# Performance work log

Measured on AMD Instinct MI355X. Metric: run time of the kernel, lower is better.

Reference implementation:

```python
import jax, jax.numpy as jnp
import numpy as np

LEAKY_ALPHA = 0.2
LN_EPS = 1e-5


def setup_inputs() -> dict:
    key = jax.random.key(0)
    ks = jax.random.split(key, 6)
    B, N, D, R, Hh, hd = 2, 2048, 128, 3, 4, 32  # head_dim = out_dim // num_heads = 128 // 4
    H = jax.random.normal(ks[0], (B, N, D), dtype=jnp.float32)
    A = jax.random.randint(ks[1], (R, B, N, N), 0, 2, dtype=jnp.int32)  # 0/1 adjacency per relation
    w_scale = float(np.sqrt(2.0 / (D + hd)))  # xavier-like
    a_scale = float(np.sqrt(2.0 / (hd + 1)))
    W = jax.random.normal(ks[2], (R, Hh, D, hd), dtype=jnp.float32) * w_scale
    a_src = jax.random.normal(ks[3], (R, Hh, hd), dtype=jnp.float32) * a_scale
    a_dst = jax.random.normal(ks[4], (R, Hh, hd), dtype=jnp.float32) * a_scale
    ln_gamma = jnp.ones((D,), dtype=jnp.float32)
    ln_beta = jnp.zeros((D,), dtype=jnp.float32)
    return {"H": H, "A": A, "W": W, "a_src": a_src, "a_dst": a_dst,
            "ln_gamma": ln_gamma, "ln_beta": ln_beta}


def reference(H, A, W, a_src, a_dst, ln_gamma, ln_beta):
    # H: [B,N,D]; A: [R,B,N,N] int; W: [R,Hh,D,hd]; a_*: [R,Hh,hd]
    R = W.shape[0]
    B, N, D = H.shape
    mask = (A > 0)[:, :, None, :, :]                    # [R,B,1,N,N]
    Wh = jnp.einsum('bnd,rhdf->rbhnf', H, W)             # [R,B,Hh,N,hd]
    e_src = jnp.einsum('rbhnf,rhf->rbhn', Wh, a_src)
    e_dst = jnp.einsum('rbhnf,rhf->rbhn', Wh, a_dst)
    e = e_src[..., :, None] + e_dst[..., None, :]        # [R,B,Hh,N,N]
    e = jax.nn.leaky_relu(e, LEAKY_ALPHA)
    all_false = ~jnp.any(mask, axis=-1, keepdims=True)   # rows with empty neighborhood
    logits = jnp.where(mask, e, -jnp.inf)
    logits = jnp.where(all_false, 0.0, logits)           # avoid NaN on empty rows
    alpha = jax.nn.softmax(logits, axis=-1)
    alpha = jnp.where(all_false, 0.0, alpha)
    # attention-weighted aggregation, mean over relations; -> [B,N,Hh,hd]
    agg = jnp.einsum('rbhij,rbhjf->bihf', alpha, Wh) / R
    out = agg.reshape(B, N, -1)                          # concat heads -> [B,N,out_dim]
    x = H + out                                          # res_proj is Identity (in_dim==out_dim); dropout in eval
    mu = jnp.mean(x, axis=-1, keepdims=True)
    var = jnp.var(x, axis=-1, keepdims=True)
    return (x - mu) / jnp.sqrt(var + LN_EPS) * ln_gamma + ln_beta
```

## Files before the change

### kernel.cpp

```cpp
#include <hip/hip_runtime.h>
#include <hip/hip_bf16.h>

#define RR 3
#define BB 2
#define NN 2048
#define DD 128
#define HH 4
#define HD 32
#define LEAKY 0.2f
#define LN_EPS 1e-5f
#define LOG2E 1.4426950408889634f

using f32x4  = __attribute__((ext_vector_type(4))) float;
using bf16x8 = __attribute__((ext_vector_type(8))) short;

__device__ __forceinline__ void gload_lds16(const void* g, void* l) {
    __builtin_amdgcn_global_load_lds(
        (const __attribute__((address_space(1))) unsigned*)g,
        (__attribute__((address_space(3))) unsigned*)l, 16, 0, 0);
}
__device__ __forceinline__ void gload_lds4(const void* g, void* l) {
    __builtin_amdgcn_global_load_lds(
        (const __attribute__((address_space(1))) unsigned*)g,
        (__attribute__((address_space(3))) unsigned*)l, 4, 0, 0);
}
__device__ __forceinline__ unsigned short bfb(float x) {
    return __builtin_bit_cast(unsigned short, __float2bfloat16(x));
}

__global__ __launch_bounds__(256) void prep_kernel(
    const float* __restrict__ H, const int* __restrict__ A,
    const float* __restrict__ W,
    const float* __restrict__ a_src, const float* __restrict__ a_dst,
    float* __restrict__ es, float* __restrict__ ed,
    __hip_bfloat16* __restrict__ whT, unsigned* __restrict__ bm)
{
    const int bid = blockIdx.x;
    const int t = threadIdx.x;

    if (bid >= 384) {
        const int cb = bid - 384;
        const int wave = cb * 4 + (t >> 6);
        const int lane = t & 63;
        const long base = (long)wave * 2048;
        const int* Ap = A + base;
        unsigned word = 0;
#pragma unroll
        for (int e = 0; e < 32; ++e) {
            const int v = Ap[e * 64 + lane];
            const unsigned long long bal = __ballot(v != 0);
            if ((lane >> 1) == e)
                word = (lane & 1) ? (unsigned)(bal >> 32) : (unsigned)bal;
        }
        bm[(base >> 5) + lane] = word;
        return;
    }

    const int rbh = bid >> 4;
    const int nch = bid & 15;
    const int h = rbh & 3;
    const int b = (rbh >> 2) & 1;
    const int r = rbh >> 3;
    const int wi = r * HH + h;
    const int w  = t >> 6;
    const int l  = t & 63;
    const int lr = l & 15;
    const int lg = l >> 4;

    const float* Wp = W + (long)wi * DD * HD;
    bf16x8 afr[2][4];
#pragma unroll
    for (int mt = 0; mt < 2; ++mt)
#pragma unroll
        for (int kt = 0; kt < 4; ++kt)
#pragma unroll
            for (int e = 0; e < 8; ++e)
                afr[mt][kt][e] = (short)bfb(Wp[(kt * 32 + lg * 8 + e) * HD + mt * 16 + lr]);

    float av[2][4], dv[2][4];
#pragma unroll
    for (int mt = 0; mt < 2; ++mt)
#pragma unroll
        for (int reg = 0; reg < 4; ++reg) {
            const int f = mt * 16 + lg * 4 + reg;
            av[mt][reg] = a_src[wi * HD + f] * LOG2E;
            dv[mt][reg] = a_dst[wi * HD + f] * LOG2E;
        }

#pragma unroll
    for (int nt = 0; nt < 2; ++nt) {
        const int ncol = nch * 128 + w * 32 + nt * 16 + lr;
        const float4* hrow4 = (const float4*)(H + ((long)b * NN + ncol) * DD);
        f32x4 acc0 = {0.f, 0.f, 0.f, 0.f};
        f32x4 acc1 = {0.f, 0.f, 0.f, 0.f};
#pragma unroll
        for (int kt = 0; kt < 4; ++kt) {
            float4 h0 = hrow4[kt * 8 + lg * 2];
            float4 h1 = hrow4[kt * 8 + lg * 2 + 1];
            bf16x8 bfr;
            bfr[0] = (short)bfb(h0.x); bfr[1] = (short)bfb(h0.y);
            bfr[2] = (short)bfb(h0.z); bfr[3] = (short)bfb(h0.w);
            bfr[4] = (short)bfb(h1.x); bfr[5] = (short)bfb(h1.y);
            bfr[6] = (short)bfb(h1.z); bfr[7] = (short)bfb(h1.w);
            acc0 = __builtin_amdgcn_mfma_f32_16x16x32_bf16(afr[0][kt], bfr, acc0, 0, 0, 0);
            acc1 = __builtin_amdgcn_mfma_f32_16x16x32_bf16(afr[1][kt], bfr, acc1, 0, 0, 0);
        }
        float s = 0.f, d = 0.f;
#pragma unroll
        for (int reg = 0; reg < 4; ++reg) {
            const int f0 = lg * 4 + reg;
            const int f1 = 16 + lg * 4 + reg;
            whT[((long)rbh * HD + f0) * NN + ncol] = __float2bfloat16(acc0[reg]);
            whT[((long)rbh * HD + f1) * NN + ncol] = __float2bfloat16(acc1[reg]);
            s = fmaf(acc0[reg], av[0][reg], s);
            s = fmaf(acc1[reg], av[1][reg], s);
            d = fmaf(acc0[reg], dv[0][reg], d);
            d = fmaf(acc1[reg], dv[1][reg], d);
        }
        s += __shfl_xor(s, 16); s += __shfl_xor(s, 32);
        d += __shfl_xor(d, 16); d += __shfl_xor(d, 32);
        if (l < 16) {
            es[(long)rbh * NN + ncol] = s;
            ed[(long)rbh * NN + ncol] = d;
        }
    }
}

__global__ __launch_bounds__(256, 3) void gat_attn_kernel(
    const unsigned* __restrict__ bm, const float* __restrict__ es,
    const float* __restrict__ ed, const __hip_bfloat16* __restrict__ whT,
    unsigned* __restrict__ num, float* __restrict__ den)
{
    const int lg = ((int)blockIdx.x % 8) * 96 + (int)blockIdx.x / 8;
    const int jh = lg & 1;
    const int it = (lg >> 1) & 15;
    const int h  = (lg >> 5) & 3;
    const int b  = (lg >> 7) & 1;
    const int r  = lg >> 8;
    const int i0 = it << 7;
    const int tid = threadIdx.x;
    const int w = tid >> 6;
    const int l = tid & 63;
    const int row = l & 15;
    const int kg  = l >> 4;
    const int f31 = l & 31;
    const int kgr = l >> 5;

    __shared__ __align__(16) short    whs[2][4][4][32][8];
    __shared__ __align__(16) unsigned bms[2][4][128];
    __shared__ __align__(16) float    eds[2][4][32];
    __shared__ float red[4];

    const int rbh = (r * BB + b) * HH + h;
    const long rbNN = (long)(r * BB + b) * NN;
    const __hip_bfloat16* whTr = whT + (long)rbh * HD * NN;
    const float* edr = ed + (long)rbh * NN;
    const int jbase = jh * (NN / 2);

#define STAGE(s, nb) do {                                                           \
        const int j0s = jbase + (s) * 128;                                          \
        gload_lds16(whTr + (long)f31 * NN + j0s + w * 32 + kgr * 8,                 \
                    &whs[nb][w][0][0][0]);                                          \
        gload_lds16(whTr + (long)f31 * NN + j0s + w * 32 + (2 + kgr) * 8,           \
                    &whs[nb][w][2][0][0]);                                          \
        gload_lds4(bm + (rbNN + i0 + l) * (NN / 32) + (j0s >> 5) + w,               \
                   &bms[nb][w][0]);                                                 \
        gload_lds4(bm + (rbNN + i0 + 64 + l) * (NN / 32) + (j0s >> 5) + w,          \
                   &bms[nb][w][64]);                                                \
        if (l < 32) gload_lds4(edr + j0s + w * 32 + l, &eds[nb][w][0]);             \
    } while (0)

    STAGE(0, 0);

    float4 m0 = ((const float4*)edr)[tid * 2];
    float4 m1 = ((const float4*)edr)[tid * 2 + 1];
    float mm = fmaxf(fmaxf(fmaxf(m0.x, m0.y), fmaxf(m0.z, m0.w)),
                     fmaxf(fmaxf(m1.x, m1.y), fmaxf(m1.z, m1.w)));
#pragma unroll
    for (int d = 1; d < 64; d <<= 1) mm = fmaxf(mm, __shfl_xor(mm, d));
    if (l == 0) red[w] = mm;
    __syncthreads();
    const float medf = fmaxf(fmaxf(red[0], red[1]), fmaxf(red[2], red[3]));

    const float esvA = es[(long)rbh * NN + i0 + w * 16 + row];
    const float esvB = es[(long)rbh * NN + i0 + 64 + w * 16 + row];
    const float xA = esvA + medf, xB = esvB + medf;
    const float MA = fmaxf(xA, LEAKY * xA), MB = fmaxf(xB, LEAKY * xB);
    const float uA = esvA - MA, vA = fmaf(LEAKY, esvA, -MA);
    const float uB = esvB - MB, vB = fmaf(LEAKY, esvB, -MB);

    f32x4 acc0A = {0,0,0,0}, acc1A = {0,0,0,0}, accDA = {0,0,0,0};
    f32x4 acc0B = {0,0,0,0}, acc1B = {0,0,0,0}, accDB = {0,0,0,0};
    bf16x8 ones;
#pragma unroll
    for (int i = 0; i < 8; ++i) ones[i] = (short)0x3F80;

    for (int s = 0; s < 8; ++s) {
        const int cb = s & 1, nb = cb ^ 1;
        if (s < 7) {
            STAGE(s + 1, nb);
            asm volatile("s_waitcnt vmcnt(5)" ::: "memory");
        } else {
            asm volatile("s_waitcnt vmcnt(0)" ::: "memory");
        }
        __builtin_amdgcn_s_barrier();
        __builtin_amdgcn_sched_barrier(0);

#pragma unroll
        for (int jc = 0; jc < 4; ++jc) {
            bf16x8 b0 = *(const bf16x8*)&whs[cb][jc][kg][row][0];
            bf16x8 b1 = *(const bf16x8*)&whs[cb][jc][kg][row + 16][0];
            float4 e0 = *(const float4*)&eds[cb][jc][kg * 8];
            float4 e1 = *(const float4*)&eds[cb][jc][kg * 8 + 4];
            const unsigned mybA = (bms[cb][jc][w * 16 + row] >> (kg * 8)) & 0xffu;
            const unsigned mybB = (bms[cb][jc][64 + w * 16 + row] >> (kg * 8)) & 0xffu;

            float ev[8];
            ev[0] = e0.x; ev[1] = e0.y; ev[2] = e0.z; ev[3] = e0.w;
            ev[4] = e1.x; ev[5] = e1.y; ev[6] = e1.z; ev[7] = e1.w;

            bf16x8 pA, pB;
#pragma unroll
            for (int c = 0; c < 8; ++c) {
                float pa = __builtin_amdgcn_exp2f(
                    fmaxf(uA + ev[c], fmaf(LEAKY, ev[c], vA)));
                float pb = __builtin_amdgcn_exp2f(
                    fmaxf(uB + ev[c], fmaf(LEAKY, ev[c], vB)));
                const int ma = ((int)(mybA << (31 - c))) >> 31;
                const int mb = ((int)(mybB << (31 - c))) >> 31;
                pa = __uint_as_float(__float_as_uint(pa) & (unsigned)ma);
                pb = __uint_as_float(__float_as_uint(pb) & (unsigned)mb);
                __hip_bfloat16 ha = __float2bfloat16(pa);
                __hip_bfloat16 hb = __float2bfloat16(pb);
                pA[c] = __builtin_bit_cast(short, ha);
                pB[c] = __builtin_bit_cast(short, hb);
            }

            acc0A = __builtin_amdgcn_mfma_f32_16x16x32_bf16(pA, b0, acc0A, 0, 0, 0);
            acc1A = __builtin_amdgcn_mfma_f32_16x16x32_bf16(pA, b1, acc1A, 0, 0, 0);
            accDA = __builtin_amdgcn_mfma_f32_16x16x32_bf16(pA, ones, accDA, 0, 0, 0);
            acc0B = __builtin_amdgcn_mfma_f32_16x16x32_bf16(pB, b0, acc0B, 0, 0, 0);
            acc1B = __builtin_amdgcn_mfma_f32_16x16x32_bf16(pB, b1, acc1B, 0, 0, 0);
            accDB = __builtin_amdgcn_mfma_f32_16x16x32_bf16(pB, ones, accDB, 0, 0, 0);
        }
        __builtin_amdgcn_s_barrier();
        __builtin_amdgcn_sched_barrier(0);
    }
#undef STAGE

    const int fcol = l & 15;
    const int pr = r * 2 + jh;
#pragma unroll
    for (int reg = 0; reg < 4; ++reg) {
        const int orow = (l >> 4) * 4 + reg;
        const long roA = (long)pr * (BB * NN) + (long)b * NN + i0 + w * 16 + orow;
        const long roB = roA + 64;
        const unsigned wa = (unsigned)bfb(acc0A[reg]) | ((unsigned)bfb(acc1A[reg]) << 16);
        const unsigned wb_ = (unsigned)bfb(acc0B[reg]) | ((unsigned)bfb(acc1B[reg]) << 16);
        num[roA * 64 + h * 16 + fcol] = wa;
        num[roB * 64 + h * 16 + fcol] = wb_;
        if (fcol == 0) {
            den[roA * HH + h] = accDA[reg];
            den[roB * HH + h] = accDB[reg];
        }
    }
}

__global__ __launch_bounds__(256) void finalize_kernel(
    const float* __restrict__ H, const unsigned* __restrict__ num,
    const float* __restrict__ den,
    const float* __restrict__ gamma, const float* __restrict__ beta,
    float* __restrict__ out)
{
    const int w = threadIdx.x >> 6;
    const int l = threadIdx.x & 63;
    const long row = (long)blockIdx.x * 4 + w;
    const int hh = l >> 4, cc = l & 15;
    const int c_lo = hh * 32 + cc, c_hi = c_lo + 16;
    const float hx = H[row * DD + c_lo];
    const float hy = H[row * DD + c_hi];

    float ax = 0.f, ay = 0.f;
#pragma unroll
    for (int r = 0; r < RR; ++r) {
        float dsum = 0.f, nx = 0.f, ny = 0.f;
#pragma unroll
        for (int j = 0; j < 2; ++j) {
            const long ro = (long)(r * 2 + j) * (BB * NN) + row;
            dsum += den[ro * HH + hh];
            const unsigned wv = num[ro * 64 + l];
            nx += __uint_as_float(wv << 16);
            ny += __uint_as_float(wv & 0xffff0000u);
        }
        const float inv = (dsum > 0.f) ? 1.0f / dsum : 0.0f;
        ax = fmaf(nx, inv, ax);
        ay = fmaf(ny, inv, ay);
    }
    const float x0 = hx + ax * (1.0f / RR);
    const float x1 = hy + ay * (1.0f / RR);
    float s = x0 + x1, q = x0 * x0 + x1 * x1;
#pragma unroll
    for (int m = 1; m < 64; m <<= 1) {
        s += __shfl_xor(s, m);
        q += __shfl_xor(q, m);
    }
    const float mu  = s * (1.0f / DD);
    const float var = q * (1.0f / DD) - mu * mu;
    const float inv = rsqrtf(var + LN_EPS);
    out[row * DD + c_lo] = (x0 - mu) * inv * gamma[c_lo] + beta[c_lo];
    out[row * DD + c_hi] = (x1 - mu) * inv * gamma[c_hi] + beta[c_hi];
}

extern "C" void kernel_launch(void* const* d_in, const int* in_sizes, int n_in,
                              void* d_out, int out_size, void* d_ws, size_t ws_size,
                              hipStream_t stream)
{
    const float* H      = (const float*)d_in[0];
    const int*   A      = (const int*)d_in[1];
    const float* W      = (const float*)d_in[2];
    const float* a_src  = (const float*)d_in[3];
    const float* a_dst  = (const float*)d_in[4];
    const float* gamma  = (const float*)d_in[5];
    const float* beta   = (const float*)d_in[6];
    float* out = (float*)d_out;

    char* ws = (char*)d_ws;
    unsigned* num = (unsigned*)ws;               ws += (size_t)RR * 2 * BB * NN * 64 * 4;
    float* den = (float*)ws;                     ws += (size_t)RR * 2 * BB * NN * HH * 4;
    float* es  = (float*)ws;                     ws += (size_t)RR * BB * HH * NN * 4;
    float* ed  = (float*)ws;                     ws += (size_t)RR * BB * HH * NN * 4;
    __hip_bfloat16* whT = (__hip_bfloat16*)ws;   ws += (size_t)RR * BB * HH * HD * NN * 2;
    unsigned* bmask = (unsigned*)ws;             ws += (size_t)RR * BB * NN * (NN / 32) * 4;

    prep_kernel<<<384 + RR * BB * NN * (NN / 32) / 256, 256, 0, stream>>>(
        H, A, W, a_src, a_dst, es, ed, whT, bmask);
    gat_attn_kernel<<<RR * BB * HH * 16 * 2, 256, 0, stream>>>(bmask, es, ed, whT, num, den);
    finalize_kernel<<<BB * NN / 4, 256, 0, stream>>>(H, num, den, gamma, beta, out);
}
```

Before: 64.55 us.

## Vectorize adjacency bitmask packing with int4 loads and interleaved bit layout

The bitmask prep now reads the int32 adjacency as int4 vectors and issues four ballots per load, so each packed word holds an interleaved set of columns instead of 32 contiguous ones. The attention kernel's staging offsets and per-lane bit extraction are rewritten to decode this interleaved layout. Each lane now reads four mask words per stage from LDS instead of one per chunk. The aim is to make the bandwidth-heavy pass over the dense adjacency cheaper through wider global loads, at the cost of more complex index arithmetic and bit decoding in the main loop.

```diff
diff --git a/kernel.cpp b/kernel.cpp
--- a/kernel.cpp
+++ b/kernel.cpp
@@ -28,6 +28,7 @@
     return __builtin_bit_cast(unsigned short, __float2bfloat16(x));
 }
 
+
 __global__ __launch_bounds__(256) void prep_kernel(
     const float* __restrict__ H, const int* __restrict__ A,
     const float* __restrict__ W,
@@ -40,19 +41,25 @@
 
     if (bid >= 384) {
         const int cb = bid - 384;
-        const int wave = cb * 4 + (t >> 6);
+        const int wv = cb * 4 + (t >> 6);
         const int lane = t & 63;
-        const long base = (long)wave * 2048;
-        const int* Ap = A + base;
-        unsigned word = 0;
-#pragma unroll
-        for (int e = 0; e < 32; ++e) {
-            const int v = Ap[e * 64 + lane];
-            const unsigned long long bal = __ballot(v != 0);
-            if ((lane >> 1) == e)
-                word = (lane & 1) ? (unsigned)(bal >> 32) : (unsigned)bal;
-        }
-        bm[(base >> 5) + lane] = word;
+        const int4* Ap = (const int4*)A;
+#pragma unroll
+        for (int e = 0; e < 8; ++e) {
+            const long chunk = (long)wv * 8 + e;
+            const int4 v = Ap[chunk * 64 + lane];
+            const unsigned long long B0 = __ballot(v.x != 0);
+            const unsigned long long B1 = __ballot(v.y != 0);
+            const unsigned long long B2 = __ballot(v.z != 0);
+            const unsigned long long B3 = __ballot(v.w != 0);
+            if (lane < 8) {
+                const unsigned long long Bq =
+                    (lane >= 6) ? B3 : (lane >= 4) ? B2 : (lane >= 2) ? B1 : B0;
+                const unsigned word = (lane & 1) ? (unsigned)(Bq >> 32)
+                                                 : (unsigned)Bq;
+                bm[chunk * 8 + lane] = word;
+            }
+        }
         return;
     }
 
@@ -159,14 +166,14 @@
 
 #define STAGE(s, nb) do {                                                           \
         const int j0s = jbase + (s) * 128;                                          \
+        const int S_ = jh * 8 + (s);                                                \
+        const int woff_ = (S_ >> 1) * 8 + (S_ & 1) + w * 2;    \
         gload_lds16(whTr + (long)f31 * NN + j0s + w * 32 + kgr * 8,                 \
                     &whs[nb][w][0][0][0]);                                          \
         gload_lds16(whTr + (long)f31 * NN + j0s + w * 32 + (2 + kgr) * 8,           \
                     &whs[nb][w][2][0][0]);                                          \
-        gload_lds4(bm + (rbNN + i0 + l) * (NN / 32) + (j0s >> 5) + w,               \
-                   &bms[nb][w][0]);                                                 \
-        gload_lds4(bm + (rbNN + i0 + 64 + l) * (NN / 32) + (j0s >> 5) + w,          \
-                   &bms[nb][w][64]);                                                \
+        gload_lds4(bm + (rbNN + i0 + l) * 64 + woff_, &bms[nb][w][0]);              \
+        gload_lds4(bm + (rbNN + i0 + 64 + l) * 64 + woff_, &bms[nb][w][64]);        \
         if (l < 32) gload_lds4(edr + j0s + w * 32 + l, &eds[nb][w][0]);             \
     } while (0)
 
@@ -194,6 +201,9 @@
     bf16x8 ones;
 #pragma unroll
     for (int i = 0; i < 8; ++i) ones[i] = (short)0x3F80;
+
+    const int kk = kg * 2;
+    const int rAi = w * 16 + row, rBi = 64 + w * 16 + row;
 
     for (int s = 0; s < 8; ++s) {
         const int cb = s & 1, nb = cb ^ 1;
@@ -206,14 +216,26 @@
         __builtin_amdgcn_s_barrier();
         __builtin_amdgcn_sched_barrier(0);
 
+        unsigned wA[4], wB[4];
+#pragma unroll
+        for (int q = 0; q < 4; ++q) {
+            wA[q] = bms[cb][q][rAi];
+            wB[q] = bms[cb][q][rBi];
+        }
+
 #pragma unroll
         for (int jc = 0; jc < 4; ++jc) {
             bf16x8 b0 = *(const bf16x8*)&whs[cb][jc][kg][row][0];
             bf16x8 b1 = *(const bf16x8*)&whs[cb][jc][kg][row + 16][0];
             float4 e0 = *(const float4*)&eds[cb][jc][kg * 8];
             float4 e1 = *(const float4*)&eds[cb][jc][kg * 8 + 4];
-            const unsigned mybA = (bms[cb][jc][w * 16 + row] >> (kg * 8)) & 0xffu;
-            const unsigned mybB = (bms[cb][jc][64 + w * 16 + row] >> (kg * 8)) & 0xffu;
+
+            unsigned uAq[4], uBq[4];
+#pragma unroll
+            for (int q = 0; q < 4; ++q) {
+                uAq[q] = wA[q] >> (jc * 8 + kk);
+                uBq[q] = wB[q] >> (jc * 8 + kk);
+            }
 
             float ev[8];
             ev[0] = e0.x; ev[1] = e0.y; ev[2] = e0.z; ev[3] = e0.w;
@@ -226,8 +248,8 @@
                     fmaxf(uA + ev[c], fmaf(LEAKY, ev[c], vA)));
                 float pb = __builtin_amdgcn_exp2f(
                     fmaxf(uB + ev[c], fmaf(LEAKY, ev[c], vB)));
-                const int ma = ((int)(mybA << (31 - c))) >> 31;
-                const int mb = ((int)(mybB << (31 - c))) >> 31;
+                const int ma = ((int)(uAq[c & 3] << (31 - (c >> 2)))) >> 31;
+                const int mb = ((int)(uBq[c & 3] << (31 - (c >> 2)))) >> 31;
                 pa = __uint_as_float(__float_as_uint(pa) & (unsigned)ma);
                 pb = __uint_as_float(__float_as_uint(pb) & (unsigned)mb);
                 __hip_bfloat16 ha = __float2bfloat16(pa);
```

New measurement: 66.14 us. +2.5%, slower.
